# Kernel tuning notes

Hardware: AMD Instinct MI355X
Metric: run time of the kernel (lower is better)

## Reference

```python
import jax, jax.numpy as jnp
import numpy as np

B, C, N, S = 4, 64, 16384, 16
DIM_OUT = 64
SCALE = DIM_OUT ** (-0.5)


def setup_inputs() -> dict:
    key = jax.random.key(0)
    ks = jax.random.split(key, 8)
    return {
        "xyz": jax.random.normal(ks[0], (B, 3, N), dtype=jnp.float32),
        "neighbor_xyz": jax.random.normal(ks[1], (B, 3, N, S), dtype=jnp.float32),
        "points": jax.random.normal(ks[2], (B, C, N), dtype=jnp.float32),
        "neighbor_points": jax.random.normal(ks[3], (B, C, N, S), dtype=jnp.float32),
        "Wk": jax.random.normal(ks[4], (C, C), dtype=jnp.float32) * 0.05,
        "Wv": jax.random.normal(ks[5], (DIM_OUT, C + 3), dtype=jnp.float32) * 0.05,
        "Wp": jax.random.normal(ks[6], (C, 4), dtype=jnp.float32) * 0.05,
        "bp": jax.random.normal(ks[7], (C,), dtype=jnp.float32) * 0.05,
    }


def reference(xyz, neighbor_xyz, points, neighbor_points, Wk, Wv, Wp, bp):
    # relative position of each neighbor: [B,3,N,S]
    tmp = xyz[:, :, :, None] - neighbor_xyz
    xyz_norm = jnp.sqrt(jnp.sum(tmp * tmp, axis=1, keepdims=True))  # [B,1,N,S]
    pos = jnp.concatenate([tmp, xyz_norm], axis=1)  # [B,4,N,S]

    # 1x1 convs == per-point channel matmuls
    pos_enc = jnp.einsum('oc,bcns->bons', Wp, pos) + bp[None, :, None, None]
    k = jnp.einsum('oc,bcns->bons', Wk, neighbor_points + pos_enc)  # [B,C,N,S]
    v_in = jnp.concatenate([neighbor_points, tmp], axis=1)  # [B,C+3,N,S]
    v = jnp.einsum('oc,bcns->bons', Wv, v_in)  # [B,dim_out,N,S]

    q = points * SCALE  # [B,C,N]
    attn = jax.nn.softmax(jnp.einsum('bcn,bcns->bns', q, k), axis=-1)  # [B,N,S]
    out = jnp.einsum('bns,bcns->bcn', attn, v)  # [B,dim_out,N]
    return out
```

## Files before the change

kernel.cpp:

```cpp
#include <hip/hip_runtime.h>
#include <math.h>

constexpr int Nn = 16384;
constexpr int ST = 68;
constexpr size_t NS = (size_t)Nn * 16;
constexpr int GPB = 4;

template <int CTRL>
__device__ __forceinline__ float dpp_f(float x) {
    return __int_as_float(
        __builtin_amdgcn_update_dpp(0, __float_as_int(x), CTRL, 0xF, 0xF, false));
}
__device__ __forceinline__ float qsum4(float v) {
    v += dpp_f<0xB1>(v);
    v += dpp_f<0x4E>(v);
    return v;
}
__device__ __forceinline__ float qmax4(float v) {
    v = fmaxf(v, dpp_f<0xB1>(v));
    v = fmaxf(v, dpp_f<0x4E>(v));
    return v;
}

#define BAR() do { asm volatile("s_waitcnt lgkmcnt(0)" ::: "memory"); \
    __builtin_amdgcn_s_barrier(); asm volatile("" ::: "memory"); } while (0)

__global__ __launch_bounds__(256, 4) void qkpp_kernel(
    const float* __restrict__ points, const float* __restrict__ Wk,
    const float* __restrict__ Wp, float* __restrict__ ws)
{
    const int tid = threadIdx.x;
    const int lane = tid & 63;
    const int q = lane >> 4;
    const int pt = blockIdx.x * 64 + (tid >> 6) * 16 + (lane & 15);
    const int b = pt >> 14;
    const int n = pt & (Nn - 1);

    float qk[16];
#pragma unroll
    for (int k = 0; k < 16; ++k) qk[k] = 0.f;

    const float* prow = points + (size_t)b * 64 * Nn + n;
    const float* wkq = Wk + 16 * q;
#pragma unroll 4
    for (int c = 0; c < 64; ++c) {
        const float qv = prow[(size_t)c * Nn];
        const float4 w0 = *(const float4*)(wkq + c * 64 + 0);
        const float4 w1 = *(const float4*)(wkq + c * 64 + 4);
        const float4 w2 = *(const float4*)(wkq + c * 64 + 8);
        const float4 w3 = *(const float4*)(wkq + c * 64 + 12);
        qk[0]  = fmaf(qv, w0.x, qk[0]);  qk[1]  = fmaf(qv, w0.y, qk[1]);
        qk[2]  = fmaf(qv, w0.z, qk[2]);  qk[3]  = fmaf(qv, w0.w, qk[3]);
        qk[4]  = fmaf(qv, w1.x, qk[4]);  qk[5]  = fmaf(qv, w1.y, qk[5]);
        qk[6]  = fmaf(qv, w1.z, qk[6]);  qk[7]  = fmaf(qv, w1.w, qk[7]);
        qk[8]  = fmaf(qv, w2.x, qk[8]);  qk[9]  = fmaf(qv, w2.y, qk[9]);
        qk[10] = fmaf(qv, w2.z, qk[10]); qk[11] = fmaf(qv, w2.w, qk[11]);
        qk[12] = fmaf(qv, w3.x, qk[12]); qk[13] = fmaf(qv, w3.y, qk[13]);
        qk[14] = fmaf(qv, w3.z, qk[14]); qk[15] = fmaf(qv, w3.w, qk[15]);
    }
#pragma unroll
    for (int k = 0; k < 16; ++k) qk[k] *= 0.125f;

    float p0 = 0.f, p1 = 0.f, p2 = 0.f, p3 = 0.f;
#pragma unroll
    for (int k = 0; k < 16; ++k) {
        const float4 wp4 = *(const float4*)(Wp + (16 * q + k) * 4);
        p0 = fmaf(qk[k], wp4.x, p0);
        p1 = fmaf(qk[k], wp4.y, p1);
        p2 = fmaf(qk[k], wp4.z, p2);
        p3 = fmaf(qk[k], wp4.w, p3);
    }
    p0 += __shfl_xor(p0, 16); p0 += __shfl_xor(p0, 32);
    p1 += __shfl_xor(p1, 16); p1 += __shfl_xor(p1, 32);
    p2 += __shfl_xor(p2, 16); p2 += __shfl_xor(p2, 32);
    p3 += __shfl_xor(p3, 16); p3 += __shfl_xor(p3, 32);

    float* orow = ws + (size_t)pt * ST + 16 * q;
    ((float4*)orow)[0] = make_float4(qk[0],  qk[1],  qk[2],  qk[3]);
    ((float4*)orow)[1] = make_float4(qk[4],  qk[5],  qk[6],  qk[7]);
    ((float4*)orow)[2] = make_float4(qk[8],  qk[9],  qk[10], qk[11]);
    ((float4*)orow)[3] = make_float4(qk[12], qk[13], qk[14], qk[15]);
    if (q == 0)
        *(float4*)(ws + (size_t)pt * ST + 64) = make_float4(p0, p1, p2, p3);
}

__global__ __launch_bounds__(256, 3) void attn_out_kernel(
    const float* __restrict__ xyz, const float* __restrict__ nxyz,
    const float* __restrict__ npts, const float* __restrict__ Wv,
    const float* __restrict__ ws, float* __restrict__ out)
{
    __shared__ float wvT[67 * 68];
    __shared__ __align__(16) float lexch[4][64][4];
    __shared__ float vbexch[67 * 17];

    const int tid = threadIdx.x;
    const int w = tid >> 6;
    const int l = tid & 63;
    const int p = l >> 2;
    const int sq = l & 3;
    const int gptbase = blockIdx.x * (16 * GPB);
    const int b = gptbase >> 14;
    const int ngbase = gptbase & (Nn - 1);

    for (int idx = tid; idx < 64 * 67; idx += 256) {
        const int o = idx / 67, c = idx - o * 67;
        wvT[c * 68 + o] = Wv[idx];
    }

    const float* npb0 = npts + ((size_t)(b * 64 + 16 * w)) * NS + (size_t)ngbase * 16 + 4 * l;

    float4 npv4[16], qq[4], nx[3], pp = make_float4(0, 0, 0, 0);
    float xx[3] = {0, 0, 0};
    nx[0] = nx[1] = nx[2] = make_float4(0, 0, 0, 0);

    {
#pragma unroll
        for (int k = 0; k < 16; ++k) npv4[k] = *(const float4*)(npb0 + (size_t)k * NS);
        const float* qrow = ws + (size_t)(gptbase + p) * ST + 16 * w;
        qq[0] = ((const float4*)qrow)[0];
        qq[1] = ((const float4*)qrow)[1];
        qq[2] = ((const float4*)qrow)[2];
        qq[3] = ((const float4*)qrow)[3];
        if (w == 3) {
            nx[0] = *(const float4*)(nxyz + ((size_t)(b * 3 + 0) * Nn + ngbase) * 16 + 4 * l);
            nx[1] = *(const float4*)(nxyz + ((size_t)(b * 3 + 1) * Nn + ngbase) * 16 + 4 * l);
            nx[2] = *(const float4*)(nxyz + ((size_t)(b * 3 + 2) * Nn + ngbase) * 16 + 4 * l);
            xx[0] = xyz[(size_t)(b * 3 + 0) * Nn + ngbase + p];
            xx[1] = xyz[(size_t)(b * 3 + 1) * Nn + ngbase + p];
            xx[2] = xyz[(size_t)(b * 3 + 2) * Nn + ngbase + p];
            pp = *(const float4*)(ws + (size_t)(gptbase + p) * ST + 64);
        }
    }

#pragma unroll
    for (int g = 0; g < GPB; ++g) {
        const int ng = ngbase + 16 * g;

        float4 d04 = make_float4(0, 0, 0, 0), d14 = d04, d24 = d04, dn4 = d04;
        if (w == 3) {
            d04 = make_float4(xx[0] - nx[0].x, xx[0] - nx[0].y, xx[0] - nx[0].z, xx[0] - nx[0].w);
            d14 = make_float4(xx[1] - nx[1].x, xx[1] - nx[1].y, xx[1] - nx[1].z, xx[1] - nx[1].w);
            d24 = make_float4(xx[2] - nx[2].x, xx[2] - nx[2].y, xx[2] - nx[2].z, xx[2] - nx[2].w);
            dn4 = make_float4(sqrtf(d04.x * d04.x + d14.x * d14.x + d24.x * d24.x),
                              sqrtf(d04.y * d04.y + d14.y * d14.y + d24.y * d24.y),
                              sqrtf(d04.z * d04.z + d14.z * d14.z + d24.z * d24.z),
                              sqrtf(d04.w * d04.w + d14.w * d14.w + d24.w * d24.w));
        }

        const float qks[16] = {qq[0].x, qq[0].y, qq[0].z, qq[0].w,
                               qq[1].x, qq[1].y, qq[1].z, qq[1].w,
                               qq[2].x, qq[2].y, qq[2].z, qq[2].w,
                               qq[3].x, qq[3].y, qq[3].z, qq[3].w};
        float4 lp = make_float4(0.f, 0.f, 0.f, 0.f);
#pragma unroll
        for (int k = 0; k < 16; ++k) {
            lp.x = fmaf(qks[k], npv4[k].x, lp.x);
            lp.y = fmaf(qks[k], npv4[k].y, lp.y);
            lp.z = fmaf(qks[k], npv4[k].z, lp.z);
            lp.w = fmaf(qks[k], npv4[k].w, lp.w);
        }
        if (w == 3) {
            lp.x += pp.x * d04.x + pp.y * d14.x + pp.z * d24.x + pp.w * dn4.x;
            lp.y += pp.x * d04.y + pp.y * d14.y + pp.z * d24.y + pp.w * dn4.y;
            lp.z += pp.x * d04.z + pp.y * d14.z + pp.z * d24.z + pp.w * dn4.z;
            lp.w += pp.x * d04.w + pp.y * d14.w + pp.z * d24.w + pp.w * dn4.w;
        }

        BAR();
        *(float4*)&lexch[w][l][0] = lp;
        BAR();
        const float4 g0 = *(const float4*)&lexch[0][l][0];
        const float4 g1 = *(const float4*)&lexch[1][l][0];
        const float4 g2 = *(const float4*)&lexch[2][l][0];
        const float4 g3 = *(const float4*)&lexch[3][l][0];
        const float4 lg = make_float4(g0.x + g1.x + g2.x + g3.x,
                                      g0.y + g1.y + g2.y + g3.y,
                                      g0.z + g1.z + g2.z + g3.z,
                                      g0.w + g1.w + g2.w + g3.w);

        float mx = fmaxf(fmaxf(lg.x, lg.y), fmaxf(lg.z, lg.w));
        mx = qmax4(mx);
        const float e0 = __expf(lg.x - mx), e1 = __expf(lg.y - mx);
        const float e2 = __expf(lg.z - mx), e3 = __expf(lg.w - mx);
        const float se = qsum4((e0 + e1) + (e2 + e3));
        const float inv = 1.0f / se;
        const float at0 = e0 * inv, at1 = e1 * inv, at2 = e2 * inv, at3 = e3 * inv;

#pragma unroll
        for (int k = 0; k < 16; ++k) {
            float v = at0 * npv4[k].x + at1 * npv4[k].y + at2 * npv4[k].z + at3 * npv4[k].w;
            v = qsum4(v);
            if (sq == (k & 3)) vbexch[(16 * w + k) * 17 + p] = v;
        }
        if (w == 3) {
            const float t0 = qsum4(at0 * d04.x + at1 * d04.y + at2 * d04.z + at3 * d04.w);
            const float t1 = qsum4(at0 * d14.x + at1 * d14.y + at2 * d14.z + at3 * d14.w);
            const float t2 = qsum4(at0 * d24.x + at1 * d24.y + at2 * d24.z + at3 * d24.w);
            if (sq == 0) vbexch[64 * 17 + p] = t0;
            else if (sq == 1) vbexch[65 * 17 + p] = t1;
            else if (sq == 2) vbexch[66 * 17 + p] = t2;
        }

        if (g + 1 < GPB) {
            const float* npb = npb0 + (size_t)(g + 1) * 256;
#pragma unroll
            for (int k = 0; k < 16; ++k) npv4[k] = *(const float4*)(npb + (size_t)k * NS);
            const float* qrow = ws + (size_t)(gptbase + 16 * (g + 1) + p) * ST + 16 * w;
            qq[0] = ((const float4*)qrow)[0];
            qq[1] = ((const float4*)qrow)[1];
            qq[2] = ((const float4*)qrow)[2];
            qq[3] = ((const float4*)qrow)[3];
            if (w == 3) {
                const int ng2 = ngbase + 16 * (g + 1);
                nx[0] = *(const float4*)(nxyz + ((size_t)(b * 3 + 0) * Nn + ng2) * 16 + 4 * l);
                nx[1] = *(const float4*)(nxyz + ((size_t)(b * 3 + 1) * Nn + ng2) * 16 + 4 * l);
                nx[2] = *(const float4*)(nxyz + ((size_t)(b * 3 + 2) * Nn + ng2) * 16 + 4 * l);
                xx[0] = xyz[(size_t)(b * 3 + 0) * Nn + ng2 + p];
                xx[1] = xyz[(size_t)(b * 3 + 1) * Nn + ng2 + p];
                xx[2] = xyz[(size_t)(b * 3 + 2) * Nn + ng2 + p];
                pp = *(const float4*)(ws + (size_t)(gptbase + 16 * (g + 1) + p) * ST + 64);
            }
        }

        BAR();

        float4 oa = make_float4(0.f, 0.f, 0.f, 0.f);
#pragma unroll
        for (int c = 0; c < 67; ++c) {
            const float vb = vbexch[c * 17 + p];
            const float4 wq = *(const float4*)&wvT[c * 68 + 16 * w + 4 * sq];
            oa.x = fmaf(vb, wq.x, oa.x);
            oa.y = fmaf(vb, wq.y, oa.y);
            oa.z = fmaf(vb, wq.z, oa.z);
            oa.w = fmaf(vb, wq.w, oa.w);
        }

        float* ob = out + ((size_t)(b * 64 + 16 * w + 4 * sq)) * Nn + ng + p;
        ob[0]              = oa.x;
        ob[(size_t)Nn]     = oa.y;
        ob[(size_t)Nn * 2] = oa.z;
        ob[(size_t)Nn * 3] = oa.w;
    }
}

extern "C" void kernel_launch(void* const* d_in, const int* in_sizes, int n_in,
                              void* d_out, int out_size, void* d_ws, size_t ws_size,
                              hipStream_t stream) {
    const float* xyz    = (const float*)d_in[0];
    const float* nxyz   = (const float*)d_in[1];
    const float* points = (const float*)d_in[2];
    const float* npts   = (const float*)d_in[3];
    const float* Wk     = (const float*)d_in[4];
    const float* Wv     = (const float*)d_in[5];
    const float* Wp     = (const float*)d_in[6];
    float* out = (float*)d_out;
    float* ws = (float*)d_ws;

    hipLaunchKernelGGL(qkpp_kernel,     dim3(1024), dim3(256), 0, stream,
                       points, Wk, Wp, ws);
    hipLaunchKernelGGL(attn_out_kernel, dim3(1024), dim3(256), 0, stream,
                       xyz, nxyz, npts, Wv, ws, out);
}
```

Baseline: 115.4 us.

## Fuse query-key projection kernel into attention kernel via LDS staging

The separate kernel that computed Wk^T·q and the Wp projection per point, and wrote them to a global workspace, is removed. Its work now runs at the start of the attention kernel, which stores the results in a new shared-memory buffer and reads them back per group. This drops one kernel launch and the global workspace write/read round-trip. In exchange it adds about 17 KB of LDS per block, which may lower occupancy, and the projection can no longer overlap with the prefetch of neighbor data.

```diff
diff --git a/kernel.cpp b/kernel.cpp
--- a/kernel.cpp
+++ b/kernel.cpp
@@ -2,7 +2,6 @@
 #include <math.h>
 
 constexpr int Nn = 16384;
-constexpr int ST = 68;
 constexpr size_t NS = (size_t)Nn * 16;
 constexpr int GPB = 4;
 
@@ -25,71 +24,14 @@
 #define BAR() do { asm volatile("s_waitcnt lgkmcnt(0)" ::: "memory"); \
     __builtin_amdgcn_s_barrier(); asm volatile("" ::: "memory"); } while (0)
 
-__global__ __launch_bounds__(256, 4) void qkpp_kernel(
-    const float* __restrict__ points, const float* __restrict__ Wk,
-    const float* __restrict__ Wp, float* __restrict__ ws)
-{
-    const int tid = threadIdx.x;
-    const int lane = tid & 63;
-    const int q = lane >> 4;
-    const int pt = blockIdx.x * 64 + (tid >> 6) * 16 + (lane & 15);
-    const int b = pt >> 14;
-    const int n = pt & (Nn - 1);
-
-    float qk[16];
-#pragma unroll
-    for (int k = 0; k < 16; ++k) qk[k] = 0.f;
-
-    const float* prow = points + (size_t)b * 64 * Nn + n;
-    const float* wkq = Wk + 16 * q;
-#pragma unroll 4
-    for (int c = 0; c < 64; ++c) {
-        const float qv = prow[(size_t)c * Nn];
-        const float4 w0 = *(const float4*)(wkq + c * 64 + 0);
-        const float4 w1 = *(const float4*)(wkq + c * 64 + 4);
-        const float4 w2 = *(const float4*)(wkq + c * 64 + 8);
-        const float4 w3 = *(const float4*)(wkq + c * 64 + 12);
-        qk[0]  = fmaf(qv, w0.x, qk[0]);  qk[1]  = fmaf(qv, w0.y, qk[1]);
-        qk[2]  = fmaf(qv, w0.z, qk[2]);  qk[3]  = fmaf(qv, w0.w, qk[3]);
-        qk[4]  = fmaf(qv, w1.x, qk[4]);  qk[5]  = fmaf(qv, w1.y, qk[5]);
-        qk[6]  = fmaf(qv, w1.z, qk[6]);  qk[7]  = fmaf(qv, w1.w, qk[7]);
-        qk[8]  = fmaf(qv, w2.x, qk[8]);  qk[9]  = fmaf(qv, w2.y, qk[9]);
-        qk[10] = fmaf(qv, w2.z, qk[10]); qk[11] = fmaf(qv, w2.w, qk[11]);
-        qk[12] = fmaf(qv, w3.x, qk[12]); qk[13] = fmaf(qv, w3.y, qk[13]);
-        qk[14] = fmaf(qv, w3.z, qk[14]); qk[15] = fmaf(qv, w3.w, qk[15]);
-    }
-#pragma unroll
-    for (int k = 0; k < 16; ++k) qk[k] *= 0.125f;
-
-    float p0 = 0.f, p1 = 0.f, p2 = 0.f, p3 = 0.f;
-#pragma unroll
-    for (int k = 0; k < 16; ++k) {
-        const float4 wp4 = *(const float4*)(Wp + (16 * q + k) * 4);
-        p0 = fmaf(qk[k], wp4.x, p0);
-        p1 = fmaf(qk[k], wp4.y, p1);
-        p2 = fmaf(qk[k], wp4.z, p2);
-        p3 = fmaf(qk[k], wp4.w, p3);
-    }
-    p0 += __shfl_xor(p0, 16); p0 += __shfl_xor(p0, 32);
-    p1 += __shfl_xor(p1, 16); p1 += __shfl_xor(p1, 32);
-    p2 += __shfl_xor(p2, 16); p2 += __shfl_xor(p2, 32);
-    p3 += __shfl_xor(p3, 16); p3 += __shfl_xor(p3, 32);
-
-    float* orow = ws + (size_t)pt * ST + 16 * q;
-    ((float4*)orow)[0] = make_float4(qk[0],  qk[1],  qk[2],  qk[3]);
-    ((float4*)orow)[1] = make_float4(qk[4],  qk[5],  qk[6],  qk[7]);
-    ((float4*)orow)[2] = make_float4(qk[8],  qk[9],  qk[10], qk[11]);
-    ((float4*)orow)[3] = make_float4(qk[12], qk[13], qk[14], qk[15]);
-    if (q == 0)
-        *(float4*)(ws + (size_t)pt * ST + 64) = make_float4(p0, p1, p2, p3);
-}
-
-__global__ __launch_bounds__(256, 3) void attn_out_kernel(
+__global__ __launch_bounds__(256, 3) void attn_fused_kernel(
     const float* __restrict__ xyz, const float* __restrict__ nxyz,
-    const float* __restrict__ npts, const float* __restrict__ Wv,
-    const float* __restrict__ ws, float* __restrict__ out)
+    const float* __restrict__ points, const float* __restrict__ npts,
+    const float* __restrict__ Wk, const float* __restrict__ Wv,
+    const float* __restrict__ Wp, float* __restrict__ out)
 {
     __shared__ float wvT[67 * 68];
+    __shared__ float qk_lds[64 * 68];
     __shared__ __align__(16) float lexch[4][64][4];
     __shared__ float vbexch[67 * 17];
 
@@ -109,18 +51,13 @@
 
     const float* npb0 = npts + ((size_t)(b * 64 + 16 * w)) * NS + (size_t)ngbase * 16 + 4 * l;
 
-    float4 npv4[16], qq[4], nx[3], pp = make_float4(0, 0, 0, 0);
+    float4 npv4[16], nx[3];
     float xx[3] = {0, 0, 0};
     nx[0] = nx[1] = nx[2] = make_float4(0, 0, 0, 0);
 
     {
 #pragma unroll
         for (int k = 0; k < 16; ++k) npv4[k] = *(const float4*)(npb0 + (size_t)k * NS);
-        const float* qrow = ws + (size_t)(gptbase + p) * ST + 16 * w;
-        qq[0] = ((const float4*)qrow)[0];
-        qq[1] = ((const float4*)qrow)[1];
-        qq[2] = ((const float4*)qrow)[2];
-        qq[3] = ((const float4*)qrow)[3];
         if (w == 3) {
             nx[0] = *(const float4*)(nxyz + ((size_t)(b * 3 + 0) * Nn + ngbase) * 16 + 4 * l);
             nx[1] = *(const float4*)(nxyz + ((size_t)(b * 3 + 1) * Nn + ngbase) * 16 + 4 * l);
@@ -128,16 +65,77 @@
             xx[0] = xyz[(size_t)(b * 3 + 0) * Nn + ngbase + p];
             xx[1] = xyz[(size_t)(b * 3 + 1) * Nn + ngbase + p];
             xx[2] = xyz[(size_t)(b * 3 + 2) * Nn + ngbase + p];
-            pp = *(const float4*)(ws + (size_t)(gptbase + p) * ST + 64);
-        }
-    }
+        }
+    }
+
+    {
+        const int quarter = l >> 4;
+        const int ptl = w * 16 + (l & 15);
+        const int n = ngbase + ptl;
+
+        float qk[16];
+#pragma unroll
+        for (int k = 0; k < 16; ++k) qk[k] = 0.f;
+
+        const float* prow = points + (size_t)b * 64 * Nn + n;
+        const float* wkq = Wk + 16 * quarter;
+#pragma unroll 4
+        for (int c = 0; c < 64; ++c) {
+            const float qv = prow[(size_t)c * Nn];
+            const float4 w0 = *(const float4*)(wkq + c * 64 + 0);
+            const float4 w1 = *(const float4*)(wkq + c * 64 + 4);
+            const float4 w2 = *(const float4*)(wkq + c * 64 + 8);
+            const float4 w3 = *(const float4*)(wkq + c * 64 + 12);
+            qk[0]  = fmaf(qv, w0.x, qk[0]);  qk[1]  = fmaf(qv, w0.y, qk[1]);
+            qk[2]  = fmaf(qv, w0.z, qk[2]);  qk[3]  = fmaf(qv, w0.w, qk[3]);
+            qk[4]  = fmaf(qv, w1.x, qk[4]);  qk[5]  = fmaf(qv, w1.y, qk[5]);
+            qk[6]  = fmaf(qv, w1.z, qk[6]);  qk[7]  = fmaf(qv, w1.w, qk[7]);
+            qk[8]  = fmaf(qv, w2.x, qk[8]);  qk[9]  = fmaf(qv, w2.y, qk[9]);
+            qk[10] = fmaf(qv, w2.z, qk[10]); qk[11] = fmaf(qv, w2.w, qk[11]);
+            qk[12] = fmaf(qv, w3.x, qk[12]); qk[13] = fmaf(qv, w3.y, qk[13]);
+            qk[14] = fmaf(qv, w3.z, qk[14]); qk[15] = fmaf(qv, w3.w, qk[15]);
+        }
+#pragma unroll
+        for (int k = 0; k < 16; ++k) qk[k] *= 0.125f;
+
+        float p0 = 0.f, p1 = 0.f, p2 = 0.f, p3 = 0.f;
+#pragma unroll
+        for (int k = 0; k < 16; ++k) {
+            const float4 wp4 = *(const float4*)(Wp + (16 * quarter + k) * 4);
+            p0 = fmaf(qk[k], wp4.x, p0);
+            p1 = fmaf(qk[k], wp4.y, p1);
+            p2 = fmaf(qk[k], wp4.z, p2);
+            p3 = fmaf(qk[k], wp4.w, p3);
+        }
+        p0 += __shfl_xor(p0, 16); p0 += __shfl_xor(p0, 32);
+        p1 += __shfl_xor(p1, 16); p1 += __shfl_xor(p1, 32);
+        p2 += __shfl_xor(p2, 16); p2 += __shfl_xor(p2, 32);
+        p3 += __shfl_xor(p3, 16); p3 += __shfl_xor(p3, 32);
+
+        float* orow = qk_lds + ptl * 68 + 16 * quarter;
+        ((float4*)orow)[0] = make_float4(qk[0],  qk[1],  qk[2],  qk[3]);
+        ((float4*)orow)[1] = make_float4(qk[4],  qk[5],  qk[6],  qk[7]);
+        ((float4*)orow)[2] = make_float4(qk[8],  qk[9],  qk[10], qk[11]);
+        ((float4*)orow)[3] = make_float4(qk[12], qk[13], qk[14], qk[15]);
+        if (quarter == 0)
+            *(float4*)(qk_lds + ptl * 68 + 64) = make_float4(p0, p1, p2, p3);
+    }
+    BAR();
 
 #pragma unroll
     for (int g = 0; g < GPB; ++g) {
         const int ng = ngbase + 16 * g;
 
+        const float* qrow = qk_lds + (16 * g + p) * 68 + 16 * w;
+        const float4 qq0 = ((const float4*)qrow)[0];
+        const float4 qq1 = ((const float4*)qrow)[1];
+        const float4 qq2 = ((const float4*)qrow)[2];
+        const float4 qq3 = ((const float4*)qrow)[3];
+        float4 pp = make_float4(0, 0, 0, 0);
+
         float4 d04 = make_float4(0, 0, 0, 0), d14 = d04, d24 = d04, dn4 = d04;
         if (w == 3) {
+            pp = *(const float4*)(qk_lds + (16 * g + p) * 68 + 64);
             d04 = make_float4(xx[0] - nx[0].x, xx[0] - nx[0].y, xx[0] - nx[0].z, xx[0] - nx[0].w);
             d14 = make_float4(xx[1] - nx[1].x, xx[1] - nx[1].y, xx[1] - nx[1].z, xx[1] - nx[1].w);
             d24 = make_float4(xx[2] - nx[2].x, xx[2] - nx[2].y, xx[2] - nx[2].z, xx[2] - nx[2].w);
@@ -147,10 +145,8 @@
                               sqrtf(d04.w * d04.w + d14.w * d14.w + d24.w * d24.w));
         }
 
-        const float qks[16] = {qq[0].x, qq[0].y, qq[0].z, qq[0].w,
-                               qq[1].x, qq[1].y, qq[1].z, qq[1].w,
-                               qq[2].x, qq[2].y, qq[2].z, qq[2].w,
-                               qq[3].x, qq[3].y, qq[3].z, qq[3].w};
+        const float qks[16] = {qq0.x, qq0.y, qq0.z, qq0.w, qq1.x, qq1.y, qq1.z, qq1.w,
+                               qq2.x, qq2.y, qq2.z, qq2.w, qq3.x, qq3.y, qq3.z, qq3.w};
         float4 lp = make_float4(0.f, 0.f, 0.f, 0.f);
 #pragma unroll
         for (int k = 0; k < 16; ++k) {
@@ -205,11 +201,6 @@
             const float* npb = npb0 + (size_t)(g + 1) * 256;
 #pragma unroll
             for (int k = 0; k < 16; ++k) npv4[k] = *(const float4*)(npb + (size_t)k * NS);
-            const float* qrow = ws + (size_t)(gptbase + 16 * (g + 1) + p) * ST + 16 * w;
-            qq[0] = ((const float4*)qrow)[0];
-            qq[1] = ((const float4*)qrow)[1];
-            qq[2] = ((const float4*)qrow)[2];
-            qq[3] = ((const float4*)qrow)[3];
             if (w == 3) {
                 const int ng2 = ngbase + 16 * (g + 1);
                 nx[0] = *(const float4*)(nxyz + ((size_t)(b * 3 + 0) * Nn + ng2) * 16 + 4 * l);
@@ -218,7 +209,6 @@
                 xx[0] = xyz[(size_t)(b * 3 + 0) * Nn + ng2 + p];
                 xx[1] = xyz[(size_t)(b * 3 + 1) * Nn + ng2 + p];
                 xx[2] = xyz[(size_t)(b * 3 + 2) * Nn + ng2 + p];
-                pp = *(const float4*)(ws + (size_t)(gptbase + 16 * (g + 1) + p) * ST + 64);
             }
         }
 
@@ -254,10 +244,7 @@
     const float* Wv     = (const float*)d_in[5];
     const float* Wp     = (const float*)d_in[6];
     float* out = (float*)d_out;
-    float* ws = (float*)d_ws;
-
-    hipLaunchKernelGGL(qkpp_kernel,     dim3(1024), dim3(256), 0, stream,
-                       points, Wk, Wp, ws);
-    hipLaunchKernelGGL(attn_out_kernel, dim3(1024), dim3(256), 0, stream,
-                       xyz, nxyz, npts, Wv, ws, out);
-}
+
+    hipLaunchKernelGGL(attn_fused_kernel, dim3(1024), dim3(256), 0, stream,
+                       xyz, nxyz, points, npts, Wk, Wv, Wp, out);
+}
```

Measured after the change: 119.2 us. 1.03x slower.
